# Optimization experiments

Measured on AMD Instinct MI355X. Metric: run time of the kernel, lower is better.

The kernel has to match this reference:

```python
import jax, jax.numpy as jnp
import numpy as np

N = 100000   # nodes
E = 800000   # edges (avg degree 8)
IN = 128     # in_dim
H = 128      # hidden_dim
L = 3        # num_layers
EPS = 1e-5   # torch LayerNorm default


def setup_inputs() -> dict:
    key = jax.random.key(0)
    ks = jax.random.split(key, 10)
    s = 0.05
    # DAG edge list: src < dst guarantees acyclicity and node N-1 is a sink.
    rng = np.random.default_rng(0)
    src = rng.integers(0, N - 1, size=E)
    dst = src + 1 + (rng.random(E) * (N - 1 - src)).astype(np.int64)
    return {
        "node_feats": jax.random.normal(ks[0], (N, IN), jnp.float32),
        "src": jnp.asarray(src, jnp.int32),
        "dst": jnp.asarray(dst, jnp.int32),
        "W_in": jax.random.normal(ks[1], (IN, H), jnp.float32) * s,
        "b_in": jnp.zeros((H,), jnp.float32),
        "Ws": jax.random.normal(ks[2], (L, H, H), jnp.float32) * s,
        "bs": jnp.zeros((L, H), jnp.float32),
        "Wn": jax.random.normal(ks[3], (L, H, H), jnp.float32) * s,
        "bn": jnp.zeros((L, H), jnp.float32),
        "Wg": jax.random.normal(ks[4], (L, 2 * H, H), jnp.float32) * s,
        "bg": jnp.zeros((L, H), jnp.float32),
        "gamma": jnp.ones((L, H), jnp.float32),
        "beta": jnp.zeros((L, H), jnp.float32),
        "W_att": jax.random.normal(ks[5], (H, H), jnp.float32) * s,
        "b_att": jnp.zeros((H,), jnp.float32),
        "W_score": jax.random.normal(ks[6], (H, 1), jnp.float32) * s,
        "b_score": jnp.zeros((1,), jnp.float32),
    }


def reference(node_feats, src, dst, W_in, b_in, Ws, bs, Wn, bn, Wg, bg,
              gamma, beta, W_att, b_att, W_score, b_score):
    n = node_feats.shape[0]
    ones_e = jnp.ones(src.shape, node_feats.dtype)
    indeg = jax.ops.segment_sum(ones_e, dst, num_segments=n)          # [N]
    has_pred = (indeg > 0).astype(node_feats.dtype)[:, None]          # [N,1]
    inv_deg = (1.0 / jnp.maximum(indeg, 1.0))[:, None]                # [N,1]
    outdeg = jax.ops.segment_sum(ones_e, src, num_segments=n)
    sink_mask = outdeg == 0                                           # [N]

    h = node_feats @ W_in + b_in                                      # [N,H]
    for i in range(Ws.shape[0]):
        hs = h @ Ws[i] + bs[i]
        # predecessor mean of layer-input h (no within-layer recurrence)
        neigh = jax.ops.segment_sum(h[src], dst, num_segments=n) * inv_deg
        hn = neigh @ Wn[i] + bn[i]
        m = hs + has_pred * hn  # nodes with no preds use m = hs only (bias too)
        gate = jax.nn.sigmoid(jnp.concatenate([h, m], axis=-1) @ Wg[i] + bg[i])
        v = gate * m + (1.0 - gate) * h
        mu = v.mean(-1, keepdims=True)
        var = ((v - mu) ** 2).mean(-1, keepdims=True)
        v = (v - mu) * jax.lax.rsqrt(var + EPS) * gamma[i] + beta[i]
        h = jax.nn.relu(v)

    # attention pooling over sink nodes only
    a = jnp.tanh(h @ W_att + b_att)
    scores = (a @ W_score)[:, 0] + b_score[0]
    scores = jnp.where(sink_mask, scores, -jnp.inf)
    w = jax.nn.softmax(scores, axis=0)  # zero weight on non-sinks
    graph_emb = (w[:, None] * h).sum(0)
    return h, graph_emb
```

## Files before the change

kernel.cpp:

```cpp
#include <hip/hip_runtime.h>
#include <cmath>

typedef unsigned short u16;
typedef unsigned int   u32;
typedef __attribute__((ext_vector_type(8))) short bf16x8;
typedef __attribute__((ext_vector_type(4))) float f32x4;
typedef __attribute__((ext_vector_type(4))) u32   u32x4;

__device__ __forceinline__ float bf2f(u16 u){
    union { u32 i; float f; } x; x.i = ((u32)u) << 16; return x.f;
}
__device__ __forceinline__ u16 f2bf(float f){
    union { float f; u32 i; } x; x.f = f;
    u32 r = x.i + 0x7fffu + ((x.i >> 16) & 1u);
    return (u16)(r >> 16);
}

__device__ __forceinline__ size_t frag_idx(int n, int k){
    int t = n >> 4, sl = n & 15, kk = k >> 5, g16 = (k >> 3) & 3, e = k & 7;
    return ((size_t)(t*4 + kk)*64 + g16*16 + sl)*8 + e;
}


__global__ void k_count(const int* __restrict__ src, const int* __restrict__ dst,
                        int* cnt, int* notsink, int* pos, int E){
    int e = blockIdx.x*256 + threadIdx.x;
    if (e < E){
        pos[e] = atomicAdd(&cnt[dst[e]], 1);
        notsink[src[e]] = 1;
    }
}

__global__ void k_sinklist(const int* __restrict__ notsink, int* sink_list,
                           int* nsink, int N){
    int i = blockIdx.x*256 + threadIdx.x;
    if (i < N && notsink[i] == 0){
        int p = atomicAdd(nsink, 1);
        sink_list[p] = i;
    }
}

__global__ void k_scan1(const int* __restrict__ in, int* blocksum, int N){
    __shared__ int sh[256];
    int tid = threadIdx.x;
    int base = blockIdx.x*1024 + tid*4;
    int s = 0;
    for (int j=0;j<4;j++){ int i = base+j; s += (i < N) ? in[i] : 0; }
    sh[tid] = s; __syncthreads();
    for (int d=128; d>0; d>>=1){ if (tid < d) sh[tid] += sh[tid+d]; __syncthreads(); }
    if (tid == 0) blocksum[blockIdx.x] = sh[0];
}

__global__ void k_scan2(int* blocksum, int nb){
    if (threadIdx.x == 0){
        int run = 0;
        for (int i=0;i<nb;i++){ int v = blocksum[i]; blocksum[i] = run; run += v; }
    }
}

__global__ void k_scan3(const int* __restrict__ in, const int* __restrict__ blockoff,
                        int* out, float* inv_deg, float* haspred, int N){
    __shared__ int sh[256];
    int tid = threadIdx.x;
    int base = blockIdx.x*1024 + tid*4;
    int e[4]; int s = 0;
    for (int j=0;j<4;j++){ int i = base+j; e[j] = (i < N) ? in[i] : 0; s += e[j]; }
    sh[tid] = s; __syncthreads();
    for (int d=1; d<256; d<<=1){
        int t = (tid >= d) ? sh[tid-d] : 0;
        __syncthreads();
        sh[tid] += t;
        __syncthreads();
    }
    int excl = sh[tid] - s + blockoff[blockIdx.x];
    for (int j=0;j<4;j++){
        int i = base+j;
        if (i < N){
            out[i] = excl; excl += e[j];
            inv_deg[i] = 1.0f / (float)(e[j] > 1 ? e[j] : 1);
            haspred[i] = e[j] > 0 ? 1.0f : 0.0f;
        }
    }
}

__global__ void k_place(const int* __restrict__ src, const int* __restrict__ dst,
                        const int* __restrict__ row_ptr, const int* __restrict__ pos,
                        int* csr_src, int E){
    int e = blockIdx.x*256 + threadIdx.x;
    if (e < E)
        csr_src[row_ptr[dst[e]] + pos[e]] = src[e];
}

__global__ void k_wt_plain(const float* __restrict__ W_in, const float* __restrict__ W_att,
                           const float* __restrict__ Ws, const float* __restrict__ Wn,
                           u16* WT_in, u16* WT_att, u16* WB){
    int i = blockIdx.x*256 + threadIdx.x;
    if (i < 32768){
        const float* srcm = (i < 16384) ? W_in : W_att;
        u16* dstm = (i < 16384) ? WT_in : WT_att;
        int w = i & 16383, n = w >> 7, k = w & 127;
        dstm[n*128 + k] = f2bf(srcm[k*128 + n]);
    } else {
        int off = i - 32768;
        int m  = off / 49152;
        int w  = off % 49152;
        int l  = w >> 14, ww = w & 16383;
        int n  = ww >> 7, k = ww & 127;
        const float* srcm = m ? Wn : Ws;
        u16* dstm = WB + ((size_t)l*2 + m)*32768;
        dstm[frag_idx(n, k)] = f2bf(srcm[(size_t)l*16384 + k*128 + n]);
    }
}

__global__ void k_wt_comp(const float* __restrict__ Ws, const float* __restrict__ Wn,
                          const float* __restrict__ Wg,
                          const float* __restrict__ bs, const float* __restrict__ bn,
                          u16* WB, float* vb){
    __shared__ float cols[2][128];
    int l = blockIdx.x / 129;
    int b = blockIdx.x % 129;
    const float* Wgb = Wg + (size_t)l*32768 + 16384;
    int tid = threadIdx.x;
    if (b == 128){
        int n = tid & 127;
        const float* bv = (tid < 128) ? (bs + l*128) : (bn + l*128);
        float acc = 0.f;
        for (int j=0;j<128;j++) acc += bv[j] * Wgb[j*128 + n];
        vb[l*256 + (tid>>7)*128 + n] = acc;
        return;
    }
    int m  = b >> 6;
    int n0 = (b & 63) * 2;
    int nn = tid >> 7, k = tid & 127;
    cols[tid>>7][tid&127] = Wgb[(size_t)(tid&127)*128 + n0 + (tid>>7)];
    __syncthreads();
    const float* A = (m ? Wn : Ws) + (size_t)l*16384;
    float acc = 0.f;
    for (int j=0;j<128;j++) acc += A[k*128 + j] * cols[nn][j];
    int n = n0 + nn;
    if (m == 0) acc += Wg[(size_t)l*32768 + k*128 + n];
    u16* dstm = WB + ((size_t)l*2 + m)*32768;
    dstm[frag_idx(128 + n, k)] = f2bf(acc);
}


__global__ void k_neigh(const u16* __restrict__ h, const int* __restrict__ row_ptr,
                        const int* __restrict__ indeg, const float* __restrict__ inv_deg,
                        const int* __restrict__ csr_src, u16* __restrict__ neigh, int N){
    int wid  = (blockIdx.x*256 + threadIdx.x) >> 6;
    int lane = threadIdx.x & 63;
    int sub = lane >> 4, sl = lane & 15;
    int node = wid*4 + sub;
    bool valid = node < N;
    int deg   = valid ? indeg[node]   : 0;
    int start = valid ? row_ptr[node] : 0;
    float acc[8] = {0.f,0.f,0.f,0.f,0.f,0.f,0.f,0.f};
    for (int e0 = 0; __any(e0 < deg); e0 += 16){
        int idx = 0;
        if (e0 + sl < deg) idx = csr_src[start + e0 + sl];
        int cnt = deg - e0;
        #pragma unroll
        for (int j = 0; j < 16; j++){
            int sidx = __shfl(idx, (sub << 4) | j);
            if (j < cnt){
                bf16x8 v = *(const bf16x8*)(h + (size_t)sidx*128 + sl*8);
                #pragma unroll
                for (int t=0;t<8;t++) acc[t] += bf2f((u16)v[t]);
            }
        }
    }
    if (valid){
        float iv = inv_deg[node];
        u16 o[8];
        #pragma unroll
        for (int t=0;t<8;t++) o[t] = f2bf(acc[t]*iv);
        *(u32x4*)(neigh + (size_t)node*128 + sl*8) = *(const u32x4*)o;
    }
}


__device__ __forceinline__ void stage_A_f32(const float* __restrict__ A, u16 (*lA)[136],
                                            int row0, int n_rows, int tid){
    #pragma unroll
    for (int i=0;i<4;i++){
        int c = i*256 + tid;
        int r = c >> 4, col8 = (c & 15) * 8;
        u16 o[8] = {0,0,0,0,0,0,0,0};
        if (row0 + r < n_rows){
            float4 v0 = *(const float4*)(A + (size_t)(row0 + r)*128 + col8);
            float4 v1 = *(const float4*)(A + (size_t)(row0 + r)*128 + col8 + 4);
            o[0]=f2bf(v0.x); o[1]=f2bf(v0.y); o[2]=f2bf(v0.z); o[3]=f2bf(v0.w);
            o[4]=f2bf(v1.x); o[5]=f2bf(v1.y); o[6]=f2bf(v1.z); o[7]=f2bf(v1.w);
        }
        *(u32x4*)&lA[r][col8] = *(const u32x4*)o;
    }
}

__device__ __forceinline__ void stage_B(const u16* __restrict__ BT, int Ks, int koff0,
                                        u16 (*lB)[136], int tid){
    #pragma unroll
    for (int i=0;i<8;i++){
        int c = i*256 + tid;
        int n = c >> 4, col8 = (c & 15) * 8;
        u32x4 v = *(const u32x4*)(BT + (size_t)n*Ks + koff0 + col8);
        *(u32x4*)&lB[n][col8] = v;
    }
}

__device__ __forceinline__ void mfma_tile(const u16 (*lA)[136], const u16 (*lB)[136],
                                          int wave, int lane, f32x4* acc){
    #pragma unroll
    for (int kk=0;kk<4;kk++){
        int koff = kk*32 + (lane >> 4) * 8;
        bf16x8 a = *(const bf16x8*)&lA[wave*16 + (lane & 15)][koff];
        #pragma unroll
        for (int t=0;t<8;t++){
            bf16x8 b = *(const bf16x8*)&lB[t*16 + (lane & 15)][koff];
            acc[t] = __builtin_amdgcn_mfma_f32_16x16x32_bf16(a, b, acc[t], 0, 0, 0);
        }
    }
}


__global__ __launch_bounds__(256) void k_gemm_in(
    const float* __restrict__ A, const u16* __restrict__ BT,
    const float* __restrict__ bias, u16* __restrict__ C, int n_rows)
{
    __shared__ u16 lA[64][136];
    __shared__ u16 lB[128][136];
    int tid = threadIdx.x, wave = tid >> 6, lane = tid & 63;
    int row0 = blockIdx.x * 64;
    f32x4 acc[8];
    #pragma unroll
    for (int t=0;t<8;t++) acc[t] = (f32x4){0.f,0.f,0.f,0.f};
    stage_A_f32(A, lA, row0, n_rows, tid);
    stage_B(BT, 128, 0, lB, tid);
    __syncthreads();
    mfma_tile(lA, lB, wave, lane, acc);

    int sl = lane & 15;
    int rbase = wave*16 + (lane >> 4)*4;
    float bc[8];
    #pragma unroll
    for (int t=0;t<8;t++) bc[t] = bias[t*16 + sl];
    for (int r=0;r<4;r++){
        int row = row0 + rbase + r;
        if (row >= n_rows) continue;
        #pragma unroll
        for (int t=0;t<8;t++)
            C[(size_t)row*128 + t*16 + sl] = f2bf(acc[t][r] + bc[t]);
    }
}


__global__ __launch_bounds__(256, 3) void k_layer(
    const u16* __restrict__ H, const u16* __restrict__ Ng,
    const u16* __restrict__ WB,
    const float* __restrict__ bs, const float* __restrict__ bn,
    const float* __restrict__ bg,
    const float* __restrict__ vb1, const float* __restrict__ vb2,
    const float* __restrict__ gamma, const float* __restrict__ beta,
    const float* __restrict__ haspred,
    u16* __restrict__ Hb, float* __restrict__ Hf, int n_rows)
{
    __shared__ u16 lH[64][132];
    __shared__ u16 lB[2][8192];
    int tid = threadIdx.x, wave = tid >> 6, lane = tid & 63;
    int sl = lane & 15, g16 = lane >> 4;
    int row0 = blockIdx.x * 64;

    int arow = row0 + wave*16 + sl;
    bool av = arow < n_rows;
    bf16x8 a1[4], a2[4];
    #pragma unroll
    for (int kk=0;kk<4;kk++){
        a1[kk] = (bf16x8){0,0,0,0,0,0,0,0};
        a2[kk] = (bf16x8){0,0,0,0,0,0,0,0};
    }
    if (av){
        #pragma unroll
        for (int kk=0;kk<4;kk++){
            a1[kk] = *(const bf16x8*)(H  + (size_t)arow*128 + kk*32 + g16*8);
            a2[kk] = *(const bf16x8*)(Ng + (size_t)arow*128 + kk*32 + g16*8);
        }
    }

    #pragma unroll
    for (int i=0;i<4;i++){
        int c = i*256 + tid;
        int r = c >> 4, col8 = (c & 15) * 8;
        u32x4 v = {0,0,0,0};
        if (row0 + r < n_rows)
            v = *(const u32x4*)(H + (size_t)(row0 + r)*128 + col8);
        *(u32x4*)&lH[r][col8] = v;
    }

    u32x4 st[4];
    #pragma unroll
    for (int i=0;i<4;i++)
        st[i] = *(const u32x4*)(WB + (size_t)(i*256 + tid)*8);
    #pragma unroll
    for (int i=0;i<4;i++)
        *(u32x4*)&lB[0][(i*256 + tid)*8] = st[i];

    f32x4 acc[16];
    #pragma unroll
    for (int t=0;t<16;t++) acc[t] = (f32x4){0.f,0.f,0.f,0.f};
    __syncthreads();

    #pragma unroll
    for (int s=0;s<8;s++){
        int cur = s & 1;
        if (s < 7){
            const u16* sp = WB + (size_t)(s+1)*8192;
            #pragma unroll
            for (int i=0;i<4;i++)
                st[i] = *(const u32x4*)(sp + (size_t)(i*256 + tid)*8);
        }
        const u16* bp = &lB[cur][lane*8];
        #pragma unroll
        for (int j=0;j<4;j++){
            #pragma unroll
            for (int kk=0;kk<4;kk++){
                bf16x8 b = *(const bf16x8*)(bp + ((j*4 + kk) << 9));
                int ai = (s & 3)*4 + j;
                acc[ai] = __builtin_amdgcn_mfma_f32_16x16x32_bf16(
                    (s >= 4) ? a2[kk] : a1[kk], b, acc[ai], 0, 0, 0);
            }
        }
        if (s < 7){
            #pragma unroll
            for (int i=0;i<4;i++)
                *(u32x4*)&lB[cur ^ 1][(i*256 + tid)*8] = st[i];
        }
        __syncthreads();
    }

    int rbase = wave*16 + g16*4;
    float bM[8], bnl[8], bG[8], vb2l[8], gam[8], bet[8];
    #pragma unroll
    for (int t=0;t<8;t++){
        int c = t*16 + sl;
        bM[t] = bs[c]; bnl[t] = bn[c];
        bG[t] = bg[c] + vb1[c]; vb2l[t] = vb2[c];
        gam[t] = gamma[c]; bet[t] = beta[c];
    }
    for (int r=0;r<4;r++){
        int row = row0 + rbase + r;
        if (row >= n_rows) continue;
        float hp = haspred[row];
        float v[8], s = 0.f;
        #pragma unroll
        for (int t=0;t<8;t++){
            int c = t*16 + sl;
            float m = acc[t][r]   + bM[t] + hp*bnl[t];
            float x = acc[t+8][r] + bG[t] + hp*vb2l[t];
            float gg = 1.f/(1.f + expf(-x));
            float hv = bf2f(lH[rbase + r][c]);
            v[t] = gg*m + (1.f - gg)*hv;
            s += v[t];
        }
        s += __shfl_xor(s,1); s += __shfl_xor(s,2); s += __shfl_xor(s,4); s += __shfl_xor(s,8);
        float mu = s * (1.f/128.f);
        float q = 0.f;
        #pragma unroll
        for (int t=0;t<8;t++){ float d = v[t]-mu; q += d*d; }
        q += __shfl_xor(q,1); q += __shfl_xor(q,2); q += __shfl_xor(q,4); q += __shfl_xor(q,8);
        float rs = rsqrtf(q*(1.f/128.f) + 1e-5f);
        #pragma unroll
        for (int t=0;t<8;t++){
            size_t idx = (size_t)row*128 + t*16 + sl;
            float o = (v[t]-mu)*rs*gam[t] + bet[t];
            o = o > 0.f ? o : 0.f;
            Hb[idx] = f2bf(o);
            if (Hf) Hf[idx] = o;
        }
    }
}


__global__ __launch_bounds__(256) void k_att_sink(
    const u16* __restrict__ H, const u16* __restrict__ BT,
    const float* __restrict__ b_att, const float* __restrict__ Wsc,
    const float* __restrict__ bsc, const int* __restrict__ sink_list,
    const int* __restrict__ nsink, float* __restrict__ scores_sink)
{
    __shared__ u16 lA[64][136];
    __shared__ u16 lB[128][136];
    int ns = *nsink;
    int tid = threadIdx.x, wave = tid >> 6, lane = tid & 63;
    int sl = lane & 15;
    stage_B(BT, 128, 0, lB, tid);
    float bac[8], wc[8];
    #pragma unroll
    for (int t=0;t<8;t++){ bac[t] = b_att[t*16 + sl]; wc[t] = Wsc[t*16 + sl]; }
    float b0 = bsc[0];
    int rbase = wave*16 + (lane >> 4)*4;

    for (int c0 = blockIdx.x*64; c0 < ns; c0 += gridDim.x*64){
        __syncthreads();
        #pragma unroll
        for (int i=0;i<4;i++){
            int c = i*256 + tid;
            int r = c >> 4, col8 = (c & 15) * 8;
            u32x4 v = {0,0,0,0};
            if (c0 + r < ns){
                int row = sink_list[c0 + r];
                v = *(const u32x4*)(H + (size_t)row*128 + col8);
            }
            *(u32x4*)&lA[r][col8] = v;
        }
        __syncthreads();
        f32x4 acc[8];
        #pragma unroll
        for (int t=0;t<8;t++) acc[t] = (f32x4){0.f,0.f,0.f,0.f};
        mfma_tile(lA, lB, wave, lane, acc);

        for (int r=0;r<4;r++){
            int i = c0 + rbase + r;
            if (i >= ns) continue;
            float p = 0.f;
            #pragma unroll
            for (int t=0;t<8;t++) p += tanhf(acc[t][r] + bac[t]) * wc[t];
            p += __shfl_xor(p,1); p += __shfl_xor(p,2); p += __shfl_xor(p,4); p += __shfl_xor(p,8);
            if (sl == 0)
                scores_sink[i] = p + b0;
        }
    }
}


__global__ void k_pool_sink(const u16* __restrict__ h, const int* __restrict__ sink_list,
                            const int* __restrict__ nsink,
                            const float* __restrict__ scores_sink,
                            float* __restrict__ out){
    __shared__ float sh[256];
    __shared__ float swg[2];
    int ns = *nsink;
    int tid = threadIdx.x;
    int col = tid & 127, grp = tid >> 7;
    float acc = 0.f, wsum = 0.f;
    for (int i = grp; i < ns; i += 2){
        float w = expf(scores_sink[i]);
        acc += w * bf2f(h[(size_t)sink_list[i]*128 + col]);
        if (col == 0) wsum += w;
    }
    sh[tid] = acc;
    if (col == 0) swg[grp] = wsum;
    __syncthreads();
    if (tid < 128) out[tid] = (sh[tid] + sh[tid+128]) / (swg[0] + swg[1]);
}


extern "C" void kernel_launch(void* const* d_in, const int* in_sizes, int n_in,
                              void* d_out, int out_size, void* d_ws, size_t ws_size,
                              hipStream_t stream)
{
    const float* node_feats = (const float*)d_in[0];
    const int* src     = (const int*)d_in[1];
    const int* dst     = (const int*)d_in[2];
    const float* W_in    = (const float*)d_in[3];
    const float* b_in    = (const float*)d_in[4];
    const float* Ws      = (const float*)d_in[5];
    const float* bs      = (const float*)d_in[6];
    const float* Wn      = (const float*)d_in[7];
    const float* bn      = (const float*)d_in[8];
    const float* Wg      = (const float*)d_in[9];
    const float* bg      = (const float*)d_in[10];
    const float* gamma   = (const float*)d_in[11];
    const float* beta    = (const float*)d_in[12];
    const float* W_att   = (const float*)d_in[13];
    const float* b_att   = (const float*)d_in[14];
    const float* W_score = (const float*)d_in[15];
    const float* b_score = (const float*)d_in[16];

    const int N = in_sizes[0] / 128;
    const int E = in_sizes[1];

    char* w = (char*)d_ws;
    auto alloc = [&](size_t bytes)->char* {
        char* p = w; w += (bytes + 255) & ~(size_t)255; return p;
    };
    u16* WT_in  = (u16*)alloc(128*128*2);
    u16* WT_att = (u16*)alloc(128*128*2);
    u16* WB     = (u16*)alloc(3*2*256*128*2);
    float* vb   = (float*)alloc(3*256*4);
    int* cnt      = (int*)alloc((size_t)N*4);
    int* notsink  = (int*)alloc((size_t)N*4);
    int* nsink    = (int*)alloc(256);
    size_t zero_bytes = (size_t)((char*)nsink + 256 - (char*)cnt);
    int* pos      = (int*)alloc((size_t)E*4);
    int* row_ptr  = (int*)alloc((size_t)N*4);
    int* blocksum = (int*)alloc(1024*4);
    int* csr_src  = (int*)alloc((size_t)E*4);
    float* inv_deg = (float*)alloc((size_t)N*4);
    float* haspred = (float*)alloc((size_t)N*4);
    int* sink_list = (int*)alloc((size_t)N*4);
    float* scores_sink = (float*)alloc((size_t)N*4);
    u16* buf0 = (u16*)alloc((size_t)N*128*2);
    u16* buf1 = (u16*)alloc((size_t)N*128*2);
    u16* bufn = (u16*)alloc((size_t)N*128*2);

    float* h_out   = (float*)d_out;
    float* emb_out = h_out + (size_t)N*128;

    hipMemsetAsync(cnt, 0, zero_bytes, stream);

    k_wt_plain<<<512, 256, 0, stream>>>(W_in, W_att, Ws, Wn, WT_in, WT_att, WB);
    k_wt_comp<<<3*129, 256, 0, stream>>>(Ws, Wn, Wg, bs, bn, WB, vb);

    k_count<<<(E+255)/256, 256, 0, stream>>>(src, dst, cnt, notsink, pos, E);
    k_sinklist<<<(N+255)/256, 256, 0, stream>>>(notsink, sink_list, nsink, N);

    int nb = (N + 1023) / 1024;
    k_scan1<<<nb, 256, 0, stream>>>(cnt, blocksum, N);
    k_scan2<<<1, 256, 0, stream>>>(blocksum, nb);
    k_scan3<<<nb, 256, 0, stream>>>(cnt, blocksum, row_ptr, inv_deg, haspred, N);
    k_place<<<(E+255)/256, 256, 0, stream>>>(src, dst, row_ptr, pos, csr_src, E);

    int gblk = (N + 63) / 64;
    int nblk = (N + 15) / 16;

    k_gemm_in<<<gblk, 256, 0, stream>>>(node_feats, WT_in, b_in, buf0, N);

    u16* hin = buf0;
    for (int i=0;i<3;i++){
        k_neigh<<<nblk, 256, 0, stream>>>(hin, row_ptr, cnt, inv_deg, csr_src, bufn, N);
        u16* hb  = (hin == buf0) ? buf1 : buf0;
        float* hf = (i == 2) ? h_out : nullptr;
        k_layer<<<gblk, 256, 0, stream>>>(hin, bufn,
                                          WB + (size_t)i*65536,
                                          bs + i*128, bn + i*128, bg + i*128,
                                          vb + i*256, vb + i*256 + 128,
                                          gamma + i*128, beta + i*128, haspred,
                                          hb, hf, N);
        hin = hb;
    }

    k_att_sink<<<8, 256, 0, stream>>>(hin, WT_att, b_att, W_score, b_score,
                                      sink_list, nsink, scores_sink);
    k_pool_sink<<<1, 256, 0, stream>>>(hin, sink_list, nsink, scores_sink, emb_out);

    (void)n_in; (void)out_size; (void)ws_size;
}
```

Baseline: 531.5 us.

## Load full layer weights into LDS once and use 128-row blocks

The layer kernel now runs with 512 threads covering 128 rows and copies the entire 128 KB packed weight block into shared memory up front. This replaces the double-buffered per-stage weight streaming and removes its seven barriers. The residual h values for the gate are now read straight from global memory instead of being staged in LDS. The cost is 128 KB of LDS per block, which limits occupancy to roughly one block per CU, and the initial weight load is no longer overlapped with MFMA work.

```diff
diff --git a/kernel.cpp b/kernel.cpp
--- a/kernel.cpp
+++ b/kernel.cpp
@@ -90,6 +90,7 @@
     if (e < E)
         csr_src[row_ptr[dst[e]] + pos[e]] = src[e];
 }
+
 
 __global__ void k_wt_plain(const float* __restrict__ W_in, const float* __restrict__ W_att,
                            const float* __restrict__ Ws, const float* __restrict__ Wn,
@@ -253,7 +254,7 @@
 }
 
 
-__global__ __launch_bounds__(256, 3) void k_layer(
+__global__ __launch_bounds__(512, 2) void k_layer(
     const u16* __restrict__ H, const u16* __restrict__ Ng,
     const u16* __restrict__ WB,
     const float* __restrict__ bs, const float* __restrict__ bn,
@@ -263,11 +264,21 @@
     const float* __restrict__ haspred,
     u16* __restrict__ Hb, float* __restrict__ Hf, int n_rows)
 {
-    __shared__ u16 lH[64][132];
-    __shared__ u16 lB[2][8192];
+    __shared__ u16 lW[65536];
     int tid = threadIdx.x, wave = tid >> 6, lane = tid & 63;
     int sl = lane & 15, g16 = lane >> 4;
-    int row0 = blockIdx.x * 64;
+    int row0 = blockIdx.x * 128;
+
+    #pragma unroll
+    for (int b=0;b<4;b++){
+        u32x4 t0[4];
+        #pragma unroll
+        for (int i=0;i<4;i++)
+            t0[i] = *(const u32x4*)(WB + (size_t)((b*4+i)*512 + tid)*8);
+        #pragma unroll
+        for (int i=0;i<4;i++)
+            *(u32x4*)&lW[((b*4+i)*512 + tid)*8] = t0[i];
+    }
 
     int arow = row0 + wave*16 + sl;
     bool av = arow < n_rows;
@@ -285,24 +296,6 @@
         }
     }
 
-    #pragma unroll
-    for (int i=0;i<4;i++){
-        int c = i*256 + tid;
-        int r = c >> 4, col8 = (c & 15) * 8;
-        u32x4 v = {0,0,0,0};
-        if (row0 + r < n_rows)
-            v = *(const u32x4*)(H + (size_t)(row0 + r)*128 + col8);
-        *(u32x4*)&lH[r][col8] = v;
-    }
-
-    u32x4 st[4];
-    #pragma unroll
-    for (int i=0;i<4;i++)
-        st[i] = *(const u32x4*)(WB + (size_t)(i*256 + tid)*8);
-    #pragma unroll
-    for (int i=0;i<4;i++)
-        *(u32x4*)&lB[0][(i*256 + tid)*8] = st[i];
-
     f32x4 acc[16];
     #pragma unroll
     for (int t=0;t<16;t++) acc[t] = (f32x4){0.f,0.f,0.f,0.f};
@@ -310,14 +303,7 @@
 
     #pragma unroll
     for (int s=0;s<8;s++){
-        int cur = s & 1;
-        if (s < 7){
-            const u16* sp = WB + (size_t)(s+1)*8192;
-            #pragma unroll
-            for (int i=0;i<4;i++)
-                st[i] = *(const u32x4*)(sp + (size_t)(i*256 + tid)*8);
-        }
-        const u16* bp = &lB[cur][lane*8];
+        const u16* bp = &lW[s*8192 + lane*8];
         #pragma unroll
         for (int j=0;j<4;j++){
             #pragma unroll
@@ -328,12 +314,6 @@
                     (s >= 4) ? a2[kk] : a1[kk], b, acc[ai], 0, 0, 0);
             }
         }
-        if (s < 7){
-            #pragma unroll
-            for (int i=0;i<4;i++)
-                *(u32x4*)&lB[cur ^ 1][(i*256 + tid)*8] = st[i];
-        }
-        __syncthreads();
     }
 
     int rbase = wave*16 + g16*4;
@@ -349,15 +329,16 @@
         int row = row0 + rbase + r;
         if (row >= n_rows) continue;
         float hp = haspred[row];
+        float hv[8];
+        #pragma unroll
+        for (int t=0;t<8;t++) hv[t] = bf2f(H[(size_t)row*128 + t*16 + sl]);
         float v[8], s = 0.f;
         #pragma unroll
         for (int t=0;t<8;t++){
-            int c = t*16 + sl;
             float m = acc[t][r]   + bM[t] + hp*bnl[t];
             float x = acc[t+8][r] + bG[t] + hp*vb2l[t];
             float gg = 1.f/(1.f + expf(-x));
-            float hv = bf2f(lH[rbase + r][c]);
-            v[t] = gg*m + (1.f - gg)*hv;
+            v[t] = gg*m + (1.f - gg)*hv[t];
             s += v[t];
         }
         s += __shfl_xor(s,1); s += __shfl_xor(s,2); s += __shfl_xor(s,4); s += __shfl_xor(s,8);
@@ -518,8 +499,9 @@
     k_scan3<<<nb, 256, 0, stream>>>(cnt, blocksum, row_ptr, inv_deg, haspred, N);
     k_place<<<(E+255)/256, 256, 0, stream>>>(src, dst, row_ptr, pos, csr_src, E);
 
-    int gblk = (N + 63) / 64;
-    int nblk = (N + 15) / 16;
+    int gblk  = (N + 63) / 64;
+    int lblk  = (N + 127) / 128;
+    int nblk  = (N + 15) / 16;
 
     k_gemm_in<<<gblk, 256, 0, stream>>>(node_feats, WT_in, b_in, buf0, N);
 
@@ -528,7 +510,7 @@
         k_neigh<<<nblk, 256, 0, stream>>>(hin, row_ptr, cnt, inv_deg, csr_src, bufn, N);
         u16* hb  = (hin == buf0) ? buf1 : buf0;
         float* hf = (i == 2) ? h_out : nullptr;
-        k_layer<<<gblk, 256, 0, stream>>>(hin, bufn,
+        k_layer<<<lblk, 512, 0, stream>>>(hin, bufn,
                                           WB + (size_t)i*65536,
                                           bs + i*128, bn + i*128, bg + i*128,
                                           vb + i*256, vb + i*256 + 128,
```

Result: slower. 553.5 us (+4.1%).

## Coalesce layer bf16 stores via LDS, skip bf16 on final layer, fold sinklist

Applied to the files above, without the earlier changes.

Non-final layers now stage the normalized bf16 output through shared memory and write it back as 16-byte coalesced row stores, replacing scattered 2-byte stores. The final layer writes only the fp32 output, dropping the redundant bf16 copy. Attention and pooling now read the fp32 output and convert it to bf16 themselves. The sink-list build is folded into the scan kernel to save one launch, at the cost of extra barriers in the layer epilogue.

```diff
diff --git a/kernel.cpp b/kernel.cpp
--- a/kernel.cpp
+++ b/kernel.cpp
@@ -28,15 +28,6 @@
     if (e < E){
         pos[e] = atomicAdd(&cnt[dst[e]], 1);
         notsink[src[e]] = 1;
-    }
-}
-
-__global__ void k_sinklist(const int* __restrict__ notsink, int* sink_list,
-                           int* nsink, int N){
-    int i = blockIdx.x*256 + threadIdx.x;
-    if (i < N && notsink[i] == 0){
-        int p = atomicAdd(nsink, 1);
-        sink_list[p] = i;
     }
 }
 
@@ -59,7 +50,9 @@
 }
 
 __global__ void k_scan3(const int* __restrict__ in, const int* __restrict__ blockoff,
-                        int* out, float* inv_deg, float* haspred, int N){
+                        const int* __restrict__ notsink,
+                        int* out, float* inv_deg, float* haspred,
+                        int* sink_list, int* nsink, int N){
     __shared__ int sh[256];
     int tid = threadIdx.x;
     int base = blockIdx.x*1024 + tid*4;
@@ -79,6 +72,10 @@
             out[i] = excl; excl += e[j];
             inv_deg[i] = 1.0f / (float)(e[j] > 1 ? e[j] : 1);
             haspred[i] = e[j] > 0 ? 1.0f : 0.0f;
+            if (notsink[i] == 0){
+                int p = atomicAdd(nsink, 1);
+                sink_list[p] = i;
+            }
         }
     }
 }
@@ -345,42 +342,84 @@
         bG[t] = bg[c] + vb1[c]; vb2l[t] = vb2[c];
         gam[t] = gamma[c]; bet[t] = beta[c];
     }
-    for (int r=0;r<4;r++){
-        int row = row0 + rbase + r;
-        if (row >= n_rows) continue;
-        float hp = haspred[row];
-        float v[8], s = 0.f;
-        #pragma unroll
-        for (int t=0;t<8;t++){
-            int c = t*16 + sl;
-            float m = acc[t][r]   + bM[t] + hp*bnl[t];
-            float x = acc[t+8][r] + bG[t] + hp*vb2l[t];
-            float gg = 1.f/(1.f + expf(-x));
-            float hv = bf2f(lH[rbase + r][c]);
-            v[t] = gg*m + (1.f - gg)*hv;
-            s += v[t];
-        }
-        s += __shfl_xor(s,1); s += __shfl_xor(s,2); s += __shfl_xor(s,4); s += __shfl_xor(s,8);
-        float mu = s * (1.f/128.f);
-        float q = 0.f;
-        #pragma unroll
-        for (int t=0;t<8;t++){ float d = v[t]-mu; q += d*d; }
-        q += __shfl_xor(q,1); q += __shfl_xor(q,2); q += __shfl_xor(q,4); q += __shfl_xor(q,8);
-        float rs = rsqrtf(q*(1.f/128.f) + 1e-5f);
-        #pragma unroll
-        for (int t=0;t<8;t++){
-            size_t idx = (size_t)row*128 + t*16 + sl;
-            float o = (v[t]-mu)*rs*gam[t] + bet[t];
-            o = o > 0.f ? o : 0.f;
-            Hb[idx] = f2bf(o);
-            if (Hf) Hf[idx] = o;
+    if (Hf){
+        for (int r=0;r<4;r++){
+            int row = row0 + rbase + r;
+            if (row >= n_rows) continue;
+            float hp = haspred[row];
+            float v[8], s = 0.f;
+            #pragma unroll
+            for (int t=0;t<8;t++){
+                int c = t*16 + sl;
+                float m = acc[t][r]   + bM[t] + hp*bnl[t];
+                float x = acc[t+8][r] + bG[t] + hp*vb2l[t];
+                float gg = 1.f/(1.f + expf(-x));
+                float hv = bf2f(lH[rbase + r][c]);
+                v[t] = gg*m + (1.f - gg)*hv;
+                s += v[t];
+            }
+            s += __shfl_xor(s,1); s += __shfl_xor(s,2); s += __shfl_xor(s,4); s += __shfl_xor(s,8);
+            float mu = s * (1.f/128.f);
+            float q = 0.f;
+            #pragma unroll
+            for (int t=0;t<8;t++){ float d = v[t]-mu; q += d*d; }
+            q += __shfl_xor(q,1); q += __shfl_xor(q,2); q += __shfl_xor(q,4); q += __shfl_xor(q,8);
+            float rs = rsqrtf(q*(1.f/128.f) + 1e-5f);
+            #pragma unroll
+            for (int t=0;t<8;t++){
+                float o = (v[t]-mu)*rs*gam[t] + bet[t];
+                Hf[(size_t)row*128 + t*16 + sl] = o > 0.f ? o : 0.f;
+            }
+        }
+    } else {
+        float ov[4][8];
+        for (int r=0;r<4;r++){
+            int row = row0 + rbase + r;
+            float hp = (row < n_rows) ? haspred[row] : 0.f;
+            float v[8], s = 0.f;
+            #pragma unroll
+            for (int t=0;t<8;t++){
+                int c = t*16 + sl;
+                float m = acc[t][r]   + bM[t] + hp*bnl[t];
+                float x = acc[t+8][r] + bG[t] + hp*vb2l[t];
+                float gg = 1.f/(1.f + expf(-x));
+                float hv = bf2f(lH[rbase + r][c]);
+                v[t] = gg*m + (1.f - gg)*hv;
+                s += v[t];
+            }
+            s += __shfl_xor(s,1); s += __shfl_xor(s,2); s += __shfl_xor(s,4); s += __shfl_xor(s,8);
+            float mu = s * (1.f/128.f);
+            float q = 0.f;
+            #pragma unroll
+            for (int t=0;t<8;t++){ float d = v[t]-mu; q += d*d; }
+            q += __shfl_xor(q,1); q += __shfl_xor(q,2); q += __shfl_xor(q,4); q += __shfl_xor(q,8);
+            float rs = rsqrtf(q*(1.f/128.f) + 1e-5f);
+            #pragma unroll
+            for (int t=0;t<8;t++){
+                float o = (v[t]-mu)*rs*gam[t] + bet[t];
+                ov[r][t] = o > 0.f ? o : 0.f;
+            }
+        }
+        __syncthreads();
+        #pragma unroll
+        for (int r=0;r<4;r++)
+            #pragma unroll
+            for (int t=0;t<8;t++)
+                lH[rbase + r][t*16 + sl] = f2bf(ov[r][t]);
+        __syncthreads();
+        #pragma unroll
+        for (int i=0;i<4;i++){
+            int c = i*256 + tid;
+            int r = c >> 4, col8 = (c & 15) * 8;
+            if (row0 + r < n_rows)
+                *(u32x4*)&Hb[(size_t)(row0 + r)*128 + col8] = *(const u32x4*)&lH[r][col8];
         }
     }
 }
 
 
 __global__ __launch_bounds__(256) void k_att_sink(
-    const u16* __restrict__ H, const u16* __restrict__ BT,
+    const float* __restrict__ Hf, const u16* __restrict__ BT,
     const float* __restrict__ b_att, const float* __restrict__ Wsc,
     const float* __restrict__ bsc, const int* __restrict__ sink_list,
     const int* __restrict__ nsink, float* __restrict__ scores_sink)
@@ -403,12 +442,15 @@
         for (int i=0;i<4;i++){
             int c = i*256 + tid;
             int r = c >> 4, col8 = (c & 15) * 8;
-            u32x4 v = {0,0,0,0};
+            u16 o[8] = {0,0,0,0,0,0,0,0};
             if (c0 + r < ns){
                 int row = sink_list[c0 + r];
-                v = *(const u32x4*)(H + (size_t)row*128 + col8);
-            }
-            *(u32x4*)&lA[r][col8] = v;
+                float4 v0 = *(const float4*)(Hf + (size_t)row*128 + col8);
+                float4 v1 = *(const float4*)(Hf + (size_t)row*128 + col8 + 4);
+                o[0]=f2bf(v0.x); o[1]=f2bf(v0.y); o[2]=f2bf(v0.z); o[3]=f2bf(v0.w);
+                o[4]=f2bf(v1.x); o[5]=f2bf(v1.y); o[6]=f2bf(v1.z); o[7]=f2bf(v1.w);
+            }
+            *(u32x4*)&lA[r][col8] = *(const u32x4*)o;
         }
         __syncthreads();
         f32x4 acc[8];
@@ -430,7 +472,7 @@
 }
 
 
-__global__ void k_pool_sink(const u16* __restrict__ h, const int* __restrict__ sink_list,
+__global__ void k_pool_sink(const float* __restrict__ Hf, const int* __restrict__ sink_list,
                             const int* __restrict__ nsink,
                             const float* __restrict__ scores_sink,
                             float* __restrict__ out){
@@ -442,7 +484,7 @@
     float acc = 0.f, wsum = 0.f;
     for (int i = grp; i < ns; i += 2){
         float w = expf(scores_sink[i]);
-        acc += w * bf2f(h[(size_t)sink_list[i]*128 + col]);
+        acc += w * Hf[(size_t)sink_list[i]*128 + col];
         if (col == 0) wsum += w;
     }
     sh[tid] = acc;
@@ -510,12 +552,12 @@
     k_wt_comp<<<3*129, 256, 0, stream>>>(Ws, Wn, Wg, bs, bn, WB, vb);
 
     k_count<<<(E+255)/256, 256, 0, stream>>>(src, dst, cnt, notsink, pos, E);
-    k_sinklist<<<(N+255)/256, 256, 0, stream>>>(notsink, sink_list, nsink, N);
 
     int nb = (N + 1023) / 1024;
     k_scan1<<<nb, 256, 0, stream>>>(cnt, blocksum, N);
     k_scan2<<<1, 256, 0, stream>>>(blocksum, nb);
-    k_scan3<<<nb, 256, 0, stream>>>(cnt, blocksum, row_ptr, inv_deg, haspred, N);
+    k_scan3<<<nb, 256, 0, stream>>>(cnt, blocksum, notsink, row_ptr, inv_deg, haspred,
+                                    sink_list, nsink, N);
     k_place<<<(E+255)/256, 256, 0, stream>>>(src, dst, row_ptr, pos, csr_src, E);
 
     int gblk = (N + 63) / 64;
@@ -537,9 +579,9 @@
         hin = hb;
     }
 
-    k_att_sink<<<8, 256, 0, stream>>>(hin, WT_att, b_att, W_score, b_score,
+    k_att_sink<<<8, 256, 0, stream>>>(h_out, WT_att, b_att, W_score, b_score,
                                       sink_list, nsink, scores_sink);
-    k_pool_sink<<<1, 256, 0, stream>>>(hin, sink_list, nsink, scores_sink, emb_out);
+    k_pool_sink<<<1, 256, 0, stream>>>(h_out, sink_list, nsink, scores_sink, emb_out);
 
     (void)n_in; (void)out_size; (void)ws_size;
 }
```

Result: no change. 531.3 us (-0.1%).
